# Performance work log

Hardware: AMD Instinct MI355X
Metric: run time of the kernel (lower is better)

Reference implementation:

```python
import jax, jax.numpy as jnp
import numpy as np

L, CH, S = 4096, 512, 64
SAMPLE_RATE = 4096.0


def setup_inputs() -> dict:
    key = jax.random.key(0)
    kx, ka, kc = jax.random.split(key, 3)
    x = jax.random.normal(kx, (L, CH), dtype=jnp.float32)
    # original init: lognegA = log(arange(1..S)) broadcast over channels; any real values work
    lognegA = jnp.broadcast_to(jnp.log(jnp.arange(1, S + 1, dtype=jnp.float32)), (CH, S)) \
        + 0.0 * jax.random.normal(ka, (CH, S), dtype=jnp.float32)
    B = jnp.ones((CH, S), dtype=jnp.float32)
    C = 0.01 * jax.random.normal(kc, (CH, S), dtype=jnp.float32)  # nn.initializers.normal() stddev=0.01
    return {"x": x, "lognegA": lognegA, "B": B, "C": C}


def reference(x, lognegA, B, C):
    length = x.shape[0]
    dt = 1.0 / SAMPLE_RATE
    A = -jnp.exp(lognegA)                         # [C, S], strictly negative
    Bd = (jnp.exp(A * dt) - 1.0) * B / A          # discretized B, [C, S]
    # Vandermonde-style kernel: Ak[l, c, s] = exp(l * A[c, s] * dt)
    Ak = jnp.exp(jnp.einsum('l,cs->lcs', jnp.arange(length, dtype=x.dtype), A * dt))
    K = jnp.einsum('cs,lcs->lc', C * Bd, Ak)      # [L, C] per-channel kernel
    # per-channel full causal convolution, truncated to length
    y = jax.vmap(jnp.convolve, in_axes=1, out_axes=1)(x, K)[:length]
    return y
```

## Files before the change

kernel.cpp:

```cpp
#include <hip/hip_runtime.h>


namespace {

constexpr int L_ = 4096;
constexpr int CH_ = 512;
constexpr int S_ = 64;
constexpr float DT = 1.0f / 4096.0f;
constexpr int SC = S_ * CH_;
constexpr int SG = 16;
constexpr int T_ = 32;
constexpr int NC_ = L_ / T_;
constexpr int CPS = 8;
constexpr int NS = NC_ / CPS;

__device__ __forceinline__ void params16(const float* __restrict__ la,
                                         const float* __restrict__ Bg,
                                         const float* __restrict__ Cg,
                                         int c, int s0, float* r, float* w) {
  const float4* lap = reinterpret_cast<const float4*>(la + c * S_ + s0);
  if (w == nullptr) {
#pragma unroll
    for (int q = 0; q < 4; ++q) {
      const float4 v = lap[q];
      const float a[4] = {v.x, v.y, v.z, v.w};
#pragma unroll
      for (int t = 0; t < 4; ++t) {
        const float A = -expf(a[t]);
        r[q * 4 + t] = expf(A * DT);
      }
    }
  } else {
    const float4* bp = reinterpret_cast<const float4*>(Bg + c * S_ + s0);
    const float4* cp = reinterpret_cast<const float4*>(Cg + c * S_ + s0);
#pragma unroll
    for (int q = 0; q < 4; ++q) {
      const float4 v = lap[q], bb = bp[q], cc = cp[q];
      const float a[4] = {v.x, v.y, v.z, v.w};
      const float bv[4] = {bb.x, bb.y, bb.z, bb.w};
      const float cv[4] = {cc.x, cc.y, cc.z, cc.w};
#pragma unroll
      for (int t = 0; t < 4; ++t) {
        const float A = -expf(a[t]);
        const float rr = expf(A * DT);
        r[q * 4 + t] = rr;
        w[q * 4 + t] = cv[t] * ((rr - 1.0f) * bv[t] / A);
      }
    }
  }
}

__global__ __launch_bounds__(256, 4)
void k_strip(const float* __restrict__ x, const float* __restrict__ la,
             float* __restrict__ P) {
  const int lane = threadIdx.x & 63;
  const int g = threadIdx.x >> 6;
  const int strip = blockIdx.x >> 3;
  const int cb = (blockIdx.x & 7) << 6;
  const int c = cb + lane;
  const int s0 = g * SG;

  float r[SG], h[SG];
  params16(la, nullptr, nullptr, c, s0, r, nullptr);
#pragma unroll
  for (int i = 0; i < SG; ++i) h[i] = 0.0f;

  const float* xp = x + (size_t)strip * CPS * T_ * CH_ + c;
  float* pp = P + (size_t)strip * CPS * SC + s0 * CH_ + c;

  for (int m = 0; m < CPS; ++m) {
#pragma unroll 8
    for (int l = 0; l < T_; ++l) {
      const float xv = xp[(m * T_ + l) * CH_];
#pragma unroll
      for (int i = 0; i < SG; ++i) h[i] = fmaf(r[i], h[i], xv);
    }
    float* pm = pp + (size_t)m * SC;
#pragma unroll
    for (int i = 0; i < SG; ++i) pm[i * CH_] = h[i];
  }
}

__global__ __launch_bounds__(256, 4)
void k_scan2(const float* __restrict__ x, const float* __restrict__ la,
             const float* __restrict__ Bg, const float* __restrict__ Cg,
             const float* __restrict__ P, float* __restrict__ y) {
  __shared__ float lds[4][8][64];

  const int lane = threadIdx.x & 63;
  const int g = threadIdx.x >> 6;
  const int k = blockIdx.x >> 3;
  const int cb = (blockIdx.x & 7) << 6;
  const int c = cb + lane;
  const int s0 = g * SG;
  const int gs = k >> 3;
  const int m = k & 7;

  float r[SG], w[SG], h[SG];
  params16(la, Bg, Cg, c, s0, r, w);

  float rT[SG], rT8[SG];
#pragma unroll
  for (int i = 0; i < SG; ++i) {
    float t = r[i];
    t *= t; t *= t; t *= t; t *= t; t *= t;
    rT[i] = t;
    t *= t; t *= t; t *= t;
    rT8[i] = t;
  }

  float G[SG];
#pragma unroll
  for (int i = 0; i < SG; ++i) G[i] = 0.0f;
  for (int gp = 0; gp < gs; ++gp) {
    const float* ap = P + ((size_t)gp * CPS + (CPS - 1)) * SC + s0 * CH_ + c;
#pragma unroll
    for (int i = 0; i < SG; ++i) G[i] = fmaf(rT8[i], G[i], ap[i * CH_]);
  }
  for (int t2 = 0; t2 < m; ++t2) {
#pragma unroll
    for (int i = 0; i < SG; ++i) G[i] *= rT[i];
  }
  if (m == 0) {
#pragma unroll
    for (int i = 0; i < SG; ++i) h[i] = G[i];
  } else {
    const float* prev = P + (size_t)(k - 1) * SC + s0 * CH_ + c;
#pragma unroll
    for (int i = 0; i < SG; ++i) h[i] = G[i] + prev[i * CH_];
  }

  const float* xp = x + (size_t)k * T_ * CH_ + c;
  float* yp = y + (size_t)k * T_ * CH_;

  for (int l = 0; l < T_; l += 8) {
    float part[8];
#pragma unroll
    for (int jj = 0; jj < 8; ++jj) {
      const float xv = xp[(l + jj) * CH_];
      float a0 = 0, a1 = 0, a2 = 0, a3 = 0;
#pragma unroll
      for (int i = 0; i < SG; i += 4) {
        h[i]     = fmaf(r[i],     h[i],     xv);
        h[i + 1] = fmaf(r[i + 1], h[i + 1], xv);
        h[i + 2] = fmaf(r[i + 2], h[i + 2], xv);
        h[i + 3] = fmaf(r[i + 3], h[i + 3], xv);
        a0 = fmaf(w[i],     h[i],     a0);
        a1 = fmaf(w[i + 1], h[i + 1], a1);
        a2 = fmaf(w[i + 2], h[i + 2], a2);
        a3 = fmaf(w[i + 3], h[i + 3], a3);
      }
      part[jj] = (a0 + a1) + (a2 + a3);
    }

#pragma unroll
    for (int jj = 0; jj < 8; ++jj) lds[g][jj][lane] = part[jj];
    __syncthreads();
#pragma unroll
    for (int p = 0; p < 2; ++p) {
      const int idx = (int)threadIdx.x + p * 256;
      const int jj = idx >> 6;
      const int ln = idx & 63;
      const float vv = (lds[0][jj][ln] + lds[1][jj][ln]) +
                       (lds[2][jj][ln] + lds[3][jj][ln]);
      yp[(size_t)(l + jj) * CH_ + cb + ln] = vv;
    }
    __syncthreads();
  }
}

__global__ __launch_bounds__(256) void k_scan_full(const float* __restrict__ x,
                                                   const float* __restrict__ la,
                                                   const float* __restrict__ Bg,
                                                   const float* __restrict__ Cg,
                                                   float* __restrict__ y) {
  __shared__ float lds[4][8][64];
  const int lane = threadIdx.x & 63;
  const int g = threadIdx.x >> 6;
  const int cb = (blockIdx.x & 7) << 6;
  const int c = cb + lane;
  const int s0 = g * SG;

  float r[SG], w[SG], h[SG];
  params16(la, Bg, Cg, c, s0, r, w);
#pragma unroll
  for (int i = 0; i < SG; ++i) h[i] = 0.0f;

  const float* xp = x + c;
  float* yp = y;

  for (int l = 0; l < L_; l += 8) {
    float part[8];
#pragma unroll
    for (int jj = 0; jj < 8; ++jj) {
      const float xv = xp[(size_t)(l + jj) * CH_];
      float a0 = 0, a1 = 0, a2 = 0, a3 = 0;
#pragma unroll
      for (int i = 0; i < SG; i += 4) {
        h[i]     = fmaf(r[i],     h[i],     xv);
        h[i + 1] = fmaf(r[i + 1], h[i + 1], xv);
        h[i + 2] = fmaf(r[i + 2], h[i + 2], xv);
        h[i + 3] = fmaf(r[i + 3], h[i + 3], xv);
        a0 = fmaf(w[i],     h[i],     a0);
        a1 = fmaf(w[i + 1], h[i + 1], a1);
        a2 = fmaf(w[i + 2], h[i + 2], a2);
        a3 = fmaf(w[i + 3], h[i + 3], a3);
      }
      part[jj] = (a0 + a1) + (a2 + a3);
    }
#pragma unroll
    for (int jj = 0; jj < 8; ++jj) lds[g][jj][lane] = part[jj];
    __syncthreads();
#pragma unroll
    for (int p = 0; p < 2; ++p) {
      const int idx = (int)threadIdx.x + p * 256;
      const int jj = idx >> 6;
      const int ln = idx & 63;
      const float vv = (lds[0][jj][ln] + lds[1][jj][ln]) +
                       (lds[2][jj][ln] + lds[3][jj][ln]);
      yp[(size_t)(l + jj) * CH_ + cb + ln] = vv;
    }
    __syncthreads();
  }
}

}

extern "C" void kernel_launch(void* const* d_in, const int* in_sizes, int n_in,
                              void* d_out, int out_size, void* d_ws, size_t ws_size,
                              hipStream_t stream) {
  const float* x = (const float*)d_in[0];
  const float* la = (const float*)d_in[1];
  const float* B = (const float*)d_in[2];
  const float* C = (const float*)d_in[3];
  float* y = (float*)d_out;
  float* P = (float*)d_ws;

  const size_t need = (size_t)NC_ * SC * sizeof(float);
  if (ws_size >= need) {
    k_strip<<<NS * 8, 256, 0, stream>>>(x, la, P);
    k_scan2<<<NC_ * 8, 256, 0, stream>>>(x, la, B, C, P, y);
  } else {
    k_scan_full<<<8, 256, 0, stream>>>(x, la, B, C, y);
  }
}
```

Measured before the change: 107.6 us.

## Replace strip-based carry scan with parallel local chunk states and prefix combine

Chunk length doubles and the first pass now computes each chunk's local end state independently, removing the sequential per-strip recurrence over eight chunks. The second pass rebuilds each chunk's incoming state by folding all earlier chunk end states with the chunk decay factor, and schedules later (longer) chunks first. This increases parallelism in the first pass at the cost of quadratic total reads of end states and a longer serial carry chain in the second pass.

```diff
diff --git a/kernel.cpp b/kernel.cpp
--- a/kernel.cpp
+++ b/kernel.cpp
@@ -9,10 +9,8 @@
 constexpr float DT = 1.0f / 4096.0f;
 constexpr int SC = S_ * CH_;
 constexpr int SG = 16;
-constexpr int T_ = 32;
+constexpr int T_ = 64;
 constexpr int NC_ = L_ / T_;
-constexpr int CPS = 8;
-constexpr int NS = NC_ / CPS;
 
 __device__ __forceinline__ void params16(const float* __restrict__ la,
                                          const float* __restrict__ Bg,
@@ -51,83 +49,64 @@
 }
 
 __global__ __launch_bounds__(256, 4)
-void k_strip(const float* __restrict__ x, const float* __restrict__ la,
-             float* __restrict__ P) {
+void k_local(const float* __restrict__ x, const float* __restrict__ la,
+             float* __restrict__ E) {
   const int lane = threadIdx.x & 63;
   const int g = threadIdx.x >> 6;
-  const int strip = blockIdx.x >> 3;
+  const int k = blockIdx.x >> 3;
+  const int c = ((blockIdx.x & 7) << 6) + lane;
+  const int s0 = g * SG;
+
+  float r[SG], h[SG];
+  params16(la, nullptr, nullptr, c, s0, r, nullptr);
+#pragma unroll
+  for (int i = 0; i < SG; ++i) h[i] = 0.0f;
+
+  const float* xp = x + (size_t)k * T_ * CH_ + c;
+#pragma unroll 8
+  for (int l = 0; l < T_; ++l) {
+    const float xv = xp[l * CH_];
+#pragma unroll
+    for (int i = 0; i < SG; ++i) h[i] = fmaf(r[i], h[i], xv);
+  }
+
+  float* ew = E + (size_t)k * SC + s0 * CH_ + c;
+#pragma unroll
+  for (int i = 0; i < SG; ++i) ew[i * CH_] = h[i];
+}
+
+__global__ __launch_bounds__(256, 4)
+void k_scan3(const float* __restrict__ x, const float* __restrict__ la,
+             const float* __restrict__ Bg, const float* __restrict__ Cg,
+             const float* __restrict__ E, float* __restrict__ y) {
+  __shared__ float lds[4][8][64];
+
+  const int lane = threadIdx.x & 63;
+  const int g = threadIdx.x >> 6;
+  const int k = (NC_ - 1) - (int)(blockIdx.x >> 3);
   const int cb = (blockIdx.x & 7) << 6;
   const int c = cb + lane;
   const int s0 = g * SG;
 
-  float r[SG], h[SG];
-  params16(la, nullptr, nullptr, c, s0, r, nullptr);
-#pragma unroll
-  for (int i = 0; i < SG; ++i) h[i] = 0.0f;
-
-  const float* xp = x + (size_t)strip * CPS * T_ * CH_ + c;
-  float* pp = P + (size_t)strip * CPS * SC + s0 * CH_ + c;
-
-  for (int m = 0; m < CPS; ++m) {
-#pragma unroll 8
-    for (int l = 0; l < T_; ++l) {
-      const float xv = xp[(m * T_ + l) * CH_];
-#pragma unroll
-      for (int i = 0; i < SG; ++i) h[i] = fmaf(r[i], h[i], xv);
-    }
-    float* pm = pp + (size_t)m * SC;
-#pragma unroll
-    for (int i = 0; i < SG; ++i) pm[i * CH_] = h[i];
-  }
-}
-
-__global__ __launch_bounds__(256, 4)
-void k_scan2(const float* __restrict__ x, const float* __restrict__ la,
-             const float* __restrict__ Bg, const float* __restrict__ Cg,
-             const float* __restrict__ P, float* __restrict__ y) {
-  __shared__ float lds[4][8][64];
-
-  const int lane = threadIdx.x & 63;
-  const int g = threadIdx.x >> 6;
-  const int k = blockIdx.x >> 3;
-  const int cb = (blockIdx.x & 7) << 6;
-  const int c = cb + lane;
-  const int s0 = g * SG;
-  const int gs = k >> 3;
-  const int m = k & 7;
-
   float r[SG], w[SG], h[SG];
   params16(la, Bg, Cg, c, s0, r, w);
 
-  float rT[SG], rT8[SG];
+  float rT[SG];
 #pragma unroll
   for (int i = 0; i < SG; ++i) {
     float t = r[i];
-    t *= t; t *= t; t *= t; t *= t; t *= t;
+    t *= t; t *= t; t *= t; t *= t; t *= t; t *= t;
     rT[i] = t;
-    t *= t; t *= t; t *= t;
-    rT8[i] = t;
-  }
-
-  float G[SG];
-#pragma unroll
-  for (int i = 0; i < SG; ++i) G[i] = 0.0f;
-  for (int gp = 0; gp < gs; ++gp) {
-    const float* ap = P + ((size_t)gp * CPS + (CPS - 1)) * SC + s0 * CH_ + c;
-#pragma unroll
-    for (int i = 0; i < SG; ++i) G[i] = fmaf(rT8[i], G[i], ap[i * CH_]);
-  }
-  for (int t2 = 0; t2 < m; ++t2) {
-#pragma unroll
-    for (int i = 0; i < SG; ++i) G[i] *= rT[i];
-  }
-  if (m == 0) {
-#pragma unroll
-    for (int i = 0; i < SG; ++i) h[i] = G[i];
-  } else {
-    const float* prev = P + (size_t)(k - 1) * SC + s0 * CH_ + c;
-#pragma unroll
-    for (int i = 0; i < SG; ++i) h[i] = G[i] + prev[i * CH_];
+  }
+
+#pragma unroll
+  for (int i = 0; i < SG; ++i) h[i] = 0.0f;
+  const float* ebase = E + s0 * CH_ + c;
+#pragma unroll 2
+  for (int j = 0; j < k; ++j) {
+    const float* ep = ebase + (size_t)j * SC;
+#pragma unroll
+    for (int i = 0; i < SG; ++i) h[i] = fmaf(rT[i], h[i], ep[i * CH_]);
   }
 
   const float* xp = x + (size_t)k * T_ * CH_ + c;
@@ -234,12 +213,12 @@
   const float* B = (const float*)d_in[2];
   const float* C = (const float*)d_in[3];
   float* y = (float*)d_out;
-  float* P = (float*)d_ws;
+  float* E = (float*)d_ws;
 
   const size_t need = (size_t)NC_ * SC * sizeof(float);
   if (ws_size >= need) {
-    k_strip<<<NS * 8, 256, 0, stream>>>(x, la, P);
-    k_scan2<<<NC_ * 8, 256, 0, stream>>>(x, la, B, C, P, y);
+    k_local<<<NC_ * 8, 256, 0, stream>>>(x, la, E);
+    k_scan3<<<NC_ * 8, 256, 0, stream>>>(x, la, B, C, E, y);
   } else {
     k_scan_full<<<8, 256, 0, stream>>>(x, la, B, C, y);
   }
```

Result: slower. 171.8 us (+59.8%).
